# Performance work log

Measured on AMD Instinct MI355X. Metric: run time of the kernel, lower is better.

## Reference

```python
import jax, jax.numpy as jnp
import numpy as np

E = 2_000_000   # edges
N = 200_000     # nodes
E_DIM = 128     # edge feature dim
G_DIM = 256     # global/graph feature dim
B = 1024        # number of graphs (batch.max()+1)
EPS = 1e-6      # torch_scatter scatter_std eps


def setup_inputs() -> dict:
    key = jax.random.key(0)
    k1, k2, k3, k4 = jax.random.split(key, 4)
    e = jax.random.normal(k1, (E, E_DIM), dtype=jnp.float32)
    e_index = jax.random.randint(k2, (2, E), 0, N, dtype=jnp.int64)
    batch = jnp.sort(jax.random.randint(k3, (N,), 0, B, dtype=jnp.int64))
    fc_w = jax.random.normal(k4, (E_DIM * 4, G_DIM), dtype=jnp.float32) * 0.02
    fc_b = jnp.zeros((G_DIM,), dtype=jnp.float32)
    return {"e_index": e_index, "e": e, "batch": batch, "fc_w": fc_w, "fc_b": fc_b}


def reference(e_index, e, batch, fc_w, fc_b):
    # graph id per edge (via target node of each edge)
    e_batch = batch[e_index[1]]  # [E]

    count = jax.ops.segment_sum(jnp.ones((e.shape[0],), e.dtype), e_batch,
                                num_segments=B)[:, None]  # [B, 1]
    s = jax.ops.segment_sum(e, e_batch, num_segments=B)    # [B, D]

    # scatter(reduce='mean'): empty segments -> 0 (divide by clamped count)
    mean = s / jnp.maximum(count, 1.0)

    # scatter min/max: torch_scatter fills empty segments with 0
    mn = jax.ops.segment_min(e, e_batch, num_segments=B)
    mx = jax.ops.segment_max(e, e_batch, num_segments=B)
    empty = count == 0.0
    mn = jnp.where(empty, 0.0, mn)
    mx = jnp.where(empty, 0.0, mx)

    # scatter_std (unbiased, matches torch_scatter composite):
    # std = sqrt(sum((x - mean)^2) / (clamp(count-1, 1) + eps))
    diff = e - mean[e_batch]                               # [E, D]
    var_sum = jax.ops.segment_sum(diff * diff, e_batch, num_segments=B)
    denom = jnp.maximum(count - 1.0, 1.0) + EPS
    std = jnp.sqrt(var_sum / denom)

    g = jnp.concatenate([mean, mn, mx, std], axis=1)       # [B, 4D]
    return g @ fc_w + fc_b                                 # [B, G_DIM]
```

## Files before the change

kernel.cpp:

```cpp
#include <hip/hip_runtime.h>
#include <math.h>

#define DIMS 128
#define GD 256
#define MAXB 1024
#define NSLOT 8
#define PARTS 4
#define NBLK 1024

typedef float vfloat4 __attribute__((ext_vector_type(4)));

__device__ __forceinline__ float4 ldnt(const float* p) {
    vfloat4 v = __builtin_nontemporal_load(reinterpret_cast<const vfloat4*>(p));
    return make_float4(v.x, v.y, v.z, v.w);
}
__device__ __forceinline__ float4 f4_add(float4 a, float4 b) {
    return make_float4(a.x + b.x, a.y + b.y, a.z + b.z, a.w + b.w);
}
__device__ __forceinline__ float4 f4_min(float4 a, float4 b) {
    return make_float4(fminf(a.x, b.x), fminf(a.y, b.y), fminf(a.z, b.z), fminf(a.w, b.w));
}
__device__ __forceinline__ float4 f4_max(float4 a, float4 b) {
    return make_float4(fmaxf(a.x, b.x), fmaxf(a.y, b.y), fmaxf(a.z, b.z), fmaxf(a.w, b.w));
}

template <int OP>
__device__ __forceinline__ float4 comb(float4 a, float4 b) {
    if (OP == 0) return f4_add(a, b);
    if (OP == 1) return f4_min(a, b);
    return f4_max(a, b);
}

template <int OP>
__device__ __forceinline__ float4 slot_reduce(float4 v, float4* red) {
    int t = threadIdx.x;
    __syncthreads();
    red[t] = v;
    __syncthreads();
    for (int off = 128; off >= 32; off >>= 1) {
        if (t < off) red[t] = comb<OP>(red[t], red[t + off]);
        __syncthreads();
    }
    return red[t & 31];
}

#define ACC(v) do { \
    sm = f4_add(sm, v); \
    sq = f4_add(sq, make_float4((v).x*(v).x, (v).y*(v).y, (v).z*(v).z, (v).w*(v).w)); \
    mn = f4_min(mn, v); mx = f4_max(mx, v); } while (0)

__global__ void __launch_bounds__(256)
hist2_kernel(const int* __restrict__ e_index, const int* __restrict__ batch,
             int E, int* __restrict__ hist2, unsigned short* __restrict__ eb) {
    __shared__ int lh[MAXB];
    for (int i = threadIdx.x; i < MAXB; i += 256) lh[i] = 0;
    __syncthreads();
    int b = blockIdx.x;
    int CH = (E + NBLK - 1) / NBLK;
    int lo = b * CH;
    int hi = min(E, lo + CH);
    for (int j = lo + threadIdx.x; j < hi; j += 256) {
        int node = e_index[E + j];
        int g = batch[node];
        eb[j] = (unsigned short)g;
        atomicAdd(&lh[g], 1);
    }
    __syncthreads();
    for (int i = threadIdx.x; i < MAXB; i += 256)
        hist2[b * MAXB + i] = lh[i];
}

__global__ void __launch_bounds__(256)
colscan_kernel(int* __restrict__ hist2, int* __restrict__ count) {
    int g = blockIdx.x;
    int t = threadIdx.x;
    int base = t * 4;
    int v[4];
#pragma unroll
    for (int i = 0; i < 4; ++i) v[i] = hist2[(base + i) * MAXB + g];
    int s0 = 0;
#pragma unroll
    for (int i = 0; i < 4; ++i) { int x = v[i]; v[i] = s0; s0 += x; }
    __shared__ int ls[256];
    ls[t] = s0;
    __syncthreads();
    for (int d = 1; d < 256; d <<= 1) {
        int x = (t >= d) ? ls[t - d] : 0;
        __syncthreads();
        ls[t] += x;
        __syncthreads();
    }
    int excl = ls[t] - s0;
#pragma unroll
    for (int i = 0; i < 4; ++i) hist2[(base + i) * MAXB + g] = excl + v[i];
    if (t == 0) count[g] = ls[255];
}

__global__ void offscan_kernel(const int* __restrict__ count, int* __restrict__ offs, int B) {
    __shared__ int tmp[MAXB];
    int t = threadIdx.x;
    int v0 = (t < B) ? count[t] : 0;
    tmp[t] = v0;
    __syncthreads();
    for (int d = 1; d < MAXB; d <<= 1) {
        int x = (t >= d) ? tmp[t - d] : 0;
        __syncthreads();
        tmp[t] += x;
        __syncthreads();
    }
    if (t < B) offs[t] = tmp[t] - v0;
}

__global__ void __launch_bounds__(256)
scatter_kernel(const unsigned short* __restrict__ eb, const int* __restrict__ hist2,
               const int* __restrict__ offs, int E, int* __restrict__ perm) {
    __shared__ int lbase[MAXB];
    __shared__ int lcur[MAXB];
    int b = blockIdx.x;
    for (int i = threadIdx.x; i < MAXB; i += 256) {
        lbase[i] = offs[i] + hist2[b * MAXB + i];
        lcur[i] = 0;
    }
    __syncthreads();
    int CH = (E + NBLK - 1) / NBLK;
    int lo = b * CH;
    int hi = min(E, lo + CH);
    for (int j = lo + threadIdx.x; j < hi; j += 256) {
        int g = eb[j];
        int r = atomicAdd(&lcur[g], 1);
        perm[lbase[g] + r] = j;
    }
}

__global__ void __launch_bounds__(256)
reduce_kernel(const float* __restrict__ e, const int* __restrict__ perm,
              const int* __restrict__ offs, const int* __restrict__ count,
              float* __restrict__ pbuf) {
    int bid = blockIdx.x;
    int g = bid >> 2;
    int p = bid & 3;
    int start = offs[g];
    int cnt = count[g];
    int chunk = (cnt + PARTS - 1) / PARTS;
    int base = start + p * chunk;
    int cnt_p = cnt - p * chunk;
    if (cnt_p > chunk) cnt_p = chunk;
    if (cnt_p < 0) cnt_p = 0;
    const int* pp = perm + base;

    int c = threadIdx.x & 31;
    int s = threadIdx.x >> 5;

    float4 sm = make_float4(0.f, 0.f, 0.f, 0.f);
    float4 sq = make_float4(0.f, 0.f, 0.f, 0.f);
    float4 mn = make_float4(INFINITY, INFINITY, INFINITY, INFINITY);
    float4 mx = make_float4(-INFINITY, -INFINITY, -INFINITY, -INFINITY);

    int i = s;
    if (i + 3 * NSLOT < cnt_p) {
        int ia0 = pp[i], ia1 = pp[i + NSLOT], ia2 = pp[i + 2 * NSLOT], ia3 = pp[i + 3 * NSLOT];
        while (true) {
            int ni = i + 4 * NSLOT;
            int na0 = 0, na1 = 0, na2 = 0, na3 = 0;
            bool nok = (ni + 3 * NSLOT < cnt_p);
            if (nok) { na0 = pp[ni]; na1 = pp[ni + NSLOT]; na2 = pp[ni + 2 * NSLOT]; na3 = pp[ni + 3 * NSLOT]; }
            float4 v0 = ldnt(e + (size_t)ia0 * DIMS + c * 4);
            float4 v1 = ldnt(e + (size_t)ia1 * DIMS + c * 4);
            float4 v2 = ldnt(e + (size_t)ia2 * DIMS + c * 4);
            float4 v3 = ldnt(e + (size_t)ia3 * DIMS + c * 4);
            ACC(v0); ACC(v1); ACC(v2); ACC(v3);
            i = ni;
            if (!nok) break;
            ia0 = na0; ia1 = na1; ia2 = na2; ia3 = na3;
        }
    }
    for (; i < cnt_p; i += NSLOT) {
        int r = pp[i];
        float4 v = ldnt(e + (size_t)r * DIMS + c * 4);
        ACC(v);
    }

    __shared__ float4 red[256];
    float4 smr = slot_reduce<0>(sm, red);
    float4 mnr = slot_reduce<1>(mn, red);
    float4 mxr = slot_reduce<2>(mx, red);
    float4 sqr = slot_reduce<0>(sq, red);

    if (threadIdx.x < 32) {
        float* row = pbuf + (size_t)bid * (4 * DIMS);
        int d0 = c * 4;
        *reinterpret_cast<float4*>(row + 0 * DIMS + d0) = smr;
        *reinterpret_cast<float4*>(row + 1 * DIMS + d0) = mnr;
        *reinterpret_cast<float4*>(row + 2 * DIMS + d0) = mxr;
        *reinterpret_cast<float4*>(row + 3 * DIMS + d0) = sqr;
    }
}

__global__ void __launch_bounds__(256)
gemm_kernel(const float* __restrict__ pbuf, const int* __restrict__ count,
            const float* __restrict__ w, const float* __restrict__ bias,
            float* __restrict__ out, int B) {
    __shared__ float gl[8 * 512];
    int r0 = blockIdx.x * 8;
    int t = threadIdx.x;
#pragma unroll
    for (int q = 0; q < 4; ++q) {
        int pair = q * 256 + t;
        int r = pair >> 7;
        int d = pair & 127;
        int g = r0 + r;
        float sm = 0.f, sq = 0.f, mnv = INFINITY, mxv = -INFINITY;
        int cnt = 0;
        if (g < B) {
            cnt = count[g];
            const float* pb = pbuf + (size_t)g * PARTS * 512;
#pragma unroll
            for (int p = 0; p < PARTS; ++p) {
                const float* row = pb + p * 512;
                sm += row[d];
                mnv = fminf(mnv, row[128 + d]);
                mxv = fmaxf(mxv, row[256 + d]);
                sq += row[384 + d];
            }
        }
        float fc = (float)cnt;
        float fcm = fmaxf(fc, 1.0f);
        float mean = sm / fcm;
        float vs = fmaxf(sq - sm * mean, 0.f);
        float sd = sqrtf(vs / (fmaxf(fc - 1.0f, 1.0f) + 1e-6f));
        if (cnt == 0) { mnv = 0.f; mxv = 0.f; }
        gl[r * 512 + 0 * 128 + d] = mean;
        gl[r * 512 + 1 * 128 + d] = mnv;
        gl[r * 512 + 2 * 128 + d] = mxv;
        gl[r * 512 + 3 * 128 + d] = sd;
    }
    __syncthreads();

    int col = t;
    float acc[8];
    float bv = bias[col];
#pragma unroll
    for (int r = 0; r < 8; ++r) acc[r] = bv;
#pragma unroll 4
    for (int k = 0; k < 512; ++k) {
        float wv = w[k * GD + col];
#pragma unroll
        for (int r = 0; r < 8; ++r) acc[r] += gl[r * 512 + k] * wv;
    }
#pragma unroll
    for (int r = 0; r < 8; ++r) {
        int rr = r0 + r;
        if (rr < B) out[(size_t)rr * GD + col] = acc[r];
    }
}

extern "C" void kernel_launch(void* const* d_in, const int* in_sizes, int n_in,
                              void* d_out, int out_size, void* d_ws, size_t ws_size,
                              hipStream_t stream) {
    const int*   e_index = (const int*)d_in[0];
    const float* e       = (const float*)d_in[1];
    const int*   batch   = (const int*)d_in[2];
    const float* fc_w    = (const float*)d_in[3];
    const float* fc_b    = (const float*)d_in[4];
    float* out = (float*)d_out;

    int E = in_sizes[1] / DIMS;
    int B = out_size / GD;

    int* hist2 = (int*)d_ws;
    int* count = hist2 + (size_t)NBLK * MAXB;
    int* offs  = count + MAXB;
    unsigned short* eb = (unsigned short*)(offs + MAXB);
    int* perm  = (int*)(eb + (((size_t)E + 1) & ~(size_t)1));
    float* pbuf = (float*)(perm + E);

    hist2_kernel<<<NBLK, 256, 0, stream>>>(e_index, batch, E, hist2, eb);
    colscan_kernel<<<MAXB, 256, 0, stream>>>(hist2, count);
    offscan_kernel<<<1, MAXB, 0, stream>>>(count, offs, B);
    scatter_kernel<<<NBLK, 256, 0, stream>>>(eb, hist2, offs, E, perm);
    reduce_kernel<<<B * PARTS, 256, 0, stream>>>(e, perm, offs, count, pbuf);
    gemm_kernel<<<(B + 7) / 8, 256, 0, stream>>>(pbuf, count, fc_w, fc_b, out, B);
}
```

Before: 279.5 us.

## Merge scans into one kernel and stage scatter through shared-memory bins

Cuts the histogram/scatter block count from 1024 to 256 and merges the column scan and offset scan into a single one-block kernel. The scatter kernel now recounts local histograms, scans them, and bins edge indices in shared memory before writing them to perm in contiguous runs per graph. This aims to save one launch and to make perm writes more coalesced. In exchange the scan runs serially in a single block, there is an extra pass over eb, and the scatter kernel uses much more shared memory. It also assumes each block's chunk fits within SCH (about 7813 edges for 2M, so it does).

```diff
diff --git a/kernel.cpp b/kernel.cpp
--- a/kernel.cpp
+++ b/kernel.cpp
@@ -6,7 +6,8 @@
 #define MAXB 1024
 #define NSLOT 8
 #define PARTS 4
-#define NBLK 1024
+#define NBLK 256
+#define SCH 8192
 
 typedef float vfloat4 __attribute__((ext_vector_type(4)));
 
@@ -67,68 +68,90 @@
     }
     __syncthreads();
     for (int i = threadIdx.x; i < MAXB; i += 256)
-        hist2[b * MAXB + i] = lh[i];
-}
-
-__global__ void __launch_bounds__(256)
-colscan_kernel(int* __restrict__ hist2, int* __restrict__ count) {
-    int g = blockIdx.x;
-    int t = threadIdx.x;
-    int base = t * 4;
-    int v[4];
-#pragma unroll
-    for (int i = 0; i < 4; ++i) v[i] = hist2[(base + i) * MAXB + g];
-    int s0 = 0;
-#pragma unroll
-    for (int i = 0; i < 4; ++i) { int x = v[i]; v[i] = s0; s0 += x; }
-    __shared__ int ls[256];
-    ls[t] = s0;
-    __syncthreads();
-    for (int d = 1; d < 256; d <<= 1) {
-        int x = (t >= d) ? ls[t - d] : 0;
-        __syncthreads();
-        ls[t] += x;
-        __syncthreads();
-    }
-    int excl = ls[t] - s0;
-#pragma unroll
-    for (int i = 0; i < 4; ++i) hist2[(base + i) * MAXB + g] = excl + v[i];
-    if (t == 0) count[g] = ls[255];
-}
-
-__global__ void offscan_kernel(const int* __restrict__ count, int* __restrict__ offs, int B) {
+        hist2[(size_t)b * MAXB + i] = lh[i];
+}
+
+__global__ void __launch_bounds__(1024)
+scanall_kernel(int* __restrict__ hist2, int* __restrict__ count, int* __restrict__ offs) {
+    int g = threadIdx.x;
+    int s = 0;
+#pragma unroll 1
+    for (int b0 = 0; b0 < NBLK; b0 += 8) {
+        int v[8];
+#pragma unroll
+        for (int i = 0; i < 8; ++i) v[i] = hist2[(size_t)(b0 + i) * MAXB + g];
+#pragma unroll
+        for (int i = 0; i < 8; ++i) { hist2[(size_t)(b0 + i) * MAXB + g] = s; s += v[i]; }
+    }
+    count[g] = s;
     __shared__ int tmp[MAXB];
-    int t = threadIdx.x;
-    int v0 = (t < B) ? count[t] : 0;
-    tmp[t] = v0;
+    tmp[g] = s;
     __syncthreads();
     for (int d = 1; d < MAXB; d <<= 1) {
-        int x = (t >= d) ? tmp[t - d] : 0;
-        __syncthreads();
-        tmp[t] += x;
-        __syncthreads();
-    }
-    if (t < B) offs[t] = tmp[t] - v0;
+        int x = (g >= d) ? tmp[g - d] : 0;
+        __syncthreads();
+        tmp[g] += x;
+        __syncthreads();
+    }
+    offs[g] = tmp[g] - s;
 }
 
 __global__ void __launch_bounds__(256)
 scatter_kernel(const unsigned short* __restrict__ eb, const int* __restrict__ hist2,
                const int* __restrict__ offs, int E, int* __restrict__ perm) {
+    __shared__ int lhist[MAXB];
+    __shared__ int lofs[MAXB];
+    __shared__ int lcur[MAXB];
     __shared__ int lbase[MAXB];
-    __shared__ int lcur[MAXB];
+    __shared__ int ws[256];
+    __shared__ int bin[SCH];
     int b = blockIdx.x;
-    for (int i = threadIdx.x; i < MAXB; i += 256) {
-        lbase[i] = offs[i] + hist2[b * MAXB + i];
-        lcur[i] = 0;
-    }
-    __syncthreads();
+    int t = threadIdx.x;
     int CH = (E + NBLK - 1) / NBLK;
     int lo = b * CH;
     int hi = min(E, lo + CH);
-    for (int j = lo + threadIdx.x; j < hi; j += 256) {
+
+    for (int i = t; i < MAXB; i += 256) {
+        lhist[i] = 0;
+        lbase[i] = offs[i] + hist2[(size_t)b * MAXB + i];
+    }
+    __syncthreads();
+    for (int j = lo + t; j < hi; j += 256) atomicAdd(&lhist[eb[j]], 1);
+    __syncthreads();
+    int base = t * 4;
+    int c0 = lhist[base + 0], c1 = lhist[base + 1], c2 = lhist[base + 2], c3 = lhist[base + 3];
+    int s0 = c0 + c1 + c2 + c3;
+    ws[t] = s0;
+    __syncthreads();
+    for (int d = 1; d < 256; d <<= 1) {
+        int x = (t >= d) ? ws[t - d] : 0;
+        __syncthreads();
+        ws[t] += x;
+        __syncthreads();
+    }
+    int excl = ws[t] - s0;
+    lofs[base + 0] = excl;
+    lofs[base + 1] = excl + c0;
+    lofs[base + 2] = excl + c0 + c1;
+    lofs[base + 3] = excl + c0 + c1 + c2;
+    lcur[base + 0] = excl;
+    lcur[base + 1] = excl + c0;
+    lcur[base + 2] = excl + c0 + c1;
+    lcur[base + 3] = excl + c0 + c1 + c2;
+    __syncthreads();
+    for (int j = lo + t; j < hi; j += 256) {
         int g = eb[j];
         int r = atomicAdd(&lcur[g], 1);
-        perm[lbase[g] + r] = j;
+        bin[r] = j;
+    }
+    __syncthreads();
+    int grp = t >> 3, sub = t & 7;
+    for (int g = grp; g < MAXB; g += 32) {
+        int sfrom = lofs[g];
+        int n = lcur[g] - sfrom;
+        int dst = lbase[g];
+        for (int k = sub; k < n; k += 8)
+            perm[dst + k] = bin[sfrom + k];
     }
 }
 
@@ -275,8 +298,7 @@
     float* pbuf = (float*)(perm + E);
 
     hist2_kernel<<<NBLK, 256, 0, stream>>>(e_index, batch, E, hist2, eb);
-    colscan_kernel<<<MAXB, 256, 0, stream>>>(hist2, count);
-    offscan_kernel<<<1, MAXB, 0, stream>>>(count, offs, B);
+    scanall_kernel<<<1, MAXB, 0, stream>>>(hist2, count, offs);
     scatter_kernel<<<NBLK, 256, 0, stream>>>(eb, hist2, offs, E, perm);
     reduce_kernel<<<B * PARTS, 256, 0, stream>>>(e, perm, offs, count, pbuf);
     gemm_kernel<<<(B + 7) / 8, 256, 0, stream>>>(pbuf, count, fc_w, fc_b, out, B);
```

Result: slower. 285.7 us (+2.2%).
